# Performance work log

Hardware: AMD Instinct MI355X
Metric: run time of the kernel (lower is better)

## Reference

```python
import jax, jax.numpy as jnp
import numpy as np

NUM_HEADS = 16
BLOCK_SIZE = 64
NUM_RANDOM_BLOCKS = 2


def _make_sparse_mask(seq_len: int) -> np.ndarray:
    # Block-diagonal pattern: token i attends to tokens in the same block.
    blk = np.arange(seq_len) // BLOCK_SIZE
    mask = blk[:, None] == blk[None, :]
    # Random extra symmetric connections (torch.randint analogue, fixed seed).
    rng = np.random.default_rng(0)
    for _ in range(NUM_RANDOM_BLOCKS):
        i = int(rng.integers(0, seq_len))
        j = int(rng.integers(0, seq_len))
        mask[i, j] = True
        mask[j, i] = True
    return mask


def setup_inputs() -> dict:
    key = jax.random.key(0)
    B, S, E = 1, 4096, 1024
    ks = jax.random.split(key, 9)
    scale = 1.0 / np.sqrt(E)
    x = jax.random.normal(ks[0], (B, S, E), dtype=jnp.float32)
    Wq = jax.random.normal(ks[1], (E, E), dtype=jnp.float32) * scale
    bq = jax.random.normal(ks[2], (E,), dtype=jnp.float32) * 0.01
    Wk = jax.random.normal(ks[3], (E, E), dtype=jnp.float32) * scale
    bk = jax.random.normal(ks[4], (E,), dtype=jnp.float32) * 0.01
    Wv = jax.random.normal(ks[5], (E, E), dtype=jnp.float32) * scale
    bv = jax.random.normal(ks[6], (E,), dtype=jnp.float32) * 0.01
    Wo = jax.random.normal(ks[7], (E, E), dtype=jnp.float32) * scale
    bo = jax.random.normal(ks[8], (E,), dtype=jnp.float32) * 0.01
    sparse_mask = jnp.asarray(_make_sparse_mask(S))
    return {"x": x, "Wq": Wq, "bq": bq, "Wk": Wk, "bk": bk,
            "Wv": Wv, "bv": bv, "Wo": Wo, "bo": bo,
            "sparse_mask": sparse_mask}


def reference(x, Wq, bq, Wk, bk, Wv, bv, Wo, bo, sparse_mask):
    B, S, E = x.shape
    H = NUM_HEADS
    D = E // H
    # Linear projections (torch Linear: y = x @ W.T + b), split into heads.
    def proj(W, b):
        y = jnp.einsum('bse,fe->bsf', x, W) + b
        return y.reshape(B, S, H, D).transpose(0, 2, 1, 3)  # [B,H,S,D]
    Q = proj(Wq, bq)
    K = proj(Wk, bk)
    V = proj(Wv, bv)
    scores = jnp.einsum('bhqd,bhkd->bhqk', Q, K) / jnp.sqrt(jnp.float32(D))
    scores = jnp.where(sparse_mask, scores, jnp.float32(-1e9))
    attn = jax.nn.softmax(scores, axis=-1)  # dropout is identity in eval
    out = jnp.einsum('bhqk,bhkd->bhqd', attn, V)
    out = out.transpose(0, 2, 1, 3).reshape(B, S, E)
    out = jnp.einsum('bse,fe->bsf', out, Wo) + bo
    return out, attn
```

## Files before the change

### kernel.cpp

```cpp
#include <hip/hip_runtime.h>
#include <cstdint>
#include <cstddef>


#define S_LEN 4096
#define EMB   1024
#define NHEAD 16
#define HDIM  64
#define NBLK  64

typedef short bf16x8 __attribute__((ext_vector_type(8)));
typedef float f32x4  __attribute__((ext_vector_type(4)));

__global__ __launch_bounds__(256) void zero_fill(uint4* __restrict__ p, size_t n)
{
  size_t i = (size_t)blockIdx.x * blockDim.x + threadIdx.x;
  const size_t stride = (size_t)gridDim.x * blockDim.x;
  const uint4 z = {0u, 0u, 0u, 0u};
  for (; i < n; i += stride) p[i] = z;
}

__device__ __forceinline__ void split1(float v, unsigned short& h, unsigned short& l)
{
  const unsigned b  = __float_as_uint(v);
  const unsigned hr = (b + 0x8000u) >> 16;
  h = (unsigned short)hr;
  const float rem = v - __uint_as_float(hr << 16);
  l = (unsigned short)((__float_as_uint(rem) + 0x8000u) >> 16);
}

__global__ __launch_bounds__(256) void split_f32_bf16(
    const float* __restrict__ in, unsigned short* __restrict__ hi,
    unsigned short* __restrict__ lo, int n4)
{
  int i = blockIdx.x * blockDim.x + threadIdx.x;
  const int stride = gridDim.x * blockDim.x;
  for (; i < n4; i += stride) {
    const float4 v = ((const float4*)in)[i];
    ushort4 h, l;
    split1(v.x, h.x, l.x);
    split1(v.y, h.y, l.y);
    split1(v.z, h.z, l.z);
    split1(v.w, h.w, l.w);
    ((ushort4*)hi)[i] = h;
    ((ushort4*)lo)[i] = l;
  }
}

__global__ __launch_bounds__(256) void gemm_mfma_split(
    const unsigned short* __restrict__ Ahi, const unsigned short* __restrict__ Alo,
    const unsigned short* __restrict__ Bhi, const unsigned short* __restrict__ Blo,
    const float* __restrict__ bias, float* __restrict__ C, int M, int N, int K)
{
  __shared__ unsigned short sAh[128 * 40];
  __shared__ unsigned short sAl[128 * 40];
  __shared__ unsigned short sBh[128 * 40];
  __shared__ unsigned short sBl[128 * 40];

  const int tid  = threadIdx.x;
  const int m0   = blockIdx.y * 128;
  const int n0   = blockIdx.x * 128;
  const int lane = tid & 63;
  const int wave = tid >> 6;
  const int wr   = wave >> 1;
  const int wc   = wave & 1;
  const int r16  = lane & 15;
  const int kc   = lane >> 4;

  const int rt = tid >> 1;
  const int ht = tid & 1;
  const unsigned short* gAh = Ahi + (size_t)(m0 + rt) * K + ht * 16;
  const unsigned short* gAl = Alo + (size_t)(m0 + rt) * K + ht * 16;
  const unsigned short* gBh = Bhi + (size_t)(n0 + rt) * K + ht * 16;
  const unsigned short* gBl = Blo + (size_t)(n0 + rt) * K + ht * 16;
  const int lds_off = rt * 40 + ht * 16;

  f32x4 acc[4][4];
  #pragma unroll
  for (int i = 0; i < 4; ++i)
    #pragma unroll
    for (int j = 0; j < 4; ++j) acc[i][j] = (f32x4){0.f, 0.f, 0.f, 0.f};

  for (int k0 = 0; k0 < K; k0 += 32) {
    const uint4 vah0 = *(const uint4*)(gAh + k0);
    const uint4 vah1 = *(const uint4*)(gAh + k0 + 8);
    const uint4 val0 = *(const uint4*)(gAl + k0);
    const uint4 val1 = *(const uint4*)(gAl + k0 + 8);
    const uint4 vbh0 = *(const uint4*)(gBh + k0);
    const uint4 vbh1 = *(const uint4*)(gBh + k0 + 8);
    const uint4 vbl0 = *(const uint4*)(gBl + k0);
    const uint4 vbl1 = *(const uint4*)(gBl + k0 + 8);

    __syncthreads();
    *(uint4*)&sAh[lds_off]     = vah0;
    *(uint4*)&sAh[lds_off + 8] = vah1;
    *(uint4*)&sAl[lds_off]     = val0;
    *(uint4*)&sAl[lds_off + 8] = val1;
    *(uint4*)&sBh[lds_off]     = vbh0;
    *(uint4*)&sBh[lds_off + 8] = vbh1;
    *(uint4*)&sBl[lds_off]     = vbl0;
    *(uint4*)&sBl[lds_off + 8] = vbl1;
    __syncthreads();

    bf16x8 ah[4], al[4], bh[4], bl[4];
    #pragma unroll
    for (int mf = 0; mf < 4; ++mf) {
      const int row = wr * 64 + mf * 16 + r16;
      ah[mf] = *(const bf16x8*)&sAh[row * 40 + kc * 8];
      al[mf] = *(const bf16x8*)&sAl[row * 40 + kc * 8];
    }
    #pragma unroll
    for (int nf = 0; nf < 4; ++nf) {
      const int col = wc * 64 + nf * 16 + r16;
      bh[nf] = *(const bf16x8*)&sBh[col * 40 + kc * 8];
      bl[nf] = *(const bf16x8*)&sBl[col * 40 + kc * 8];
    }
    #pragma unroll
    for (int mf = 0; mf < 4; ++mf)
      #pragma unroll
      for (int nf = 0; nf < 4; ++nf) {
        acc[mf][nf] = __builtin_amdgcn_mfma_f32_16x16x32_bf16(ah[mf], bh[nf], acc[mf][nf], 0, 0, 0);
        acc[mf][nf] = __builtin_amdgcn_mfma_f32_16x16x32_bf16(ah[mf], bl[nf], acc[mf][nf], 0, 0, 0);
        acc[mf][nf] = __builtin_amdgcn_mfma_f32_16x16x32_bf16(al[mf], bh[nf], acc[mf][nf], 0, 0, 0);
      }
  }

  const int fq = lane >> 4;
  #pragma unroll
  for (int mf = 0; mf < 4; ++mf) {
    #pragma unroll
    for (int nf = 0; nf < 4; ++nf) {
      const int col = n0 + wc * 64 + nf * 16 + r16;
      const float bb = bias[col];
      #pragma unroll
      for (int v = 0; v < 4; ++v) {
        const int row = m0 + wr * 64 + mf * 16 + fq * 4 + v;
        C[(size_t)row * N + col] = acc[mf][nf][v] + bb;
      }
    }
  }
}

struct GemmPtrs {
  const float* W[3];
  const float* b[3];
  float* C[3];
};

__global__ __launch_bounds__(256) void gemm_bt_f32(const float* __restrict__ A,
                                                   GemmPtrs p, int M, int N, int K)
{
  const int z = blockIdx.z;
  const float* __restrict__ W    = p.W[z];
  const float* __restrict__ bias = p.b[z];
  float* __restrict__ C          = p.C[z];

  __shared__ float As[16][132];
  __shared__ float Bs[16][132];

  const int tid = threadIdx.x;
  const int tx = tid & 15;
  const int ty = tid >> 4;
  const int m0 = blockIdx.y * 128;
  const int n0 = blockIdx.x * 128;
  const int r0 = tid >> 2;
  const int c4 = tid & 3;

  const float* Ap  = A + (size_t)(m0 + r0) * K + c4 * 4;
  const float* Ap2 = Ap + (size_t)64 * K;
  const float* Wp  = W + (size_t)(n0 + r0) * K + c4 * 4;
  const float* Wp2 = Wp + (size_t)64 * K;

  float acc[8][8];
  #pragma unroll
  for (int i = 0; i < 8; ++i)
    #pragma unroll
    for (int j = 0; j < 8; ++j) acc[i][j] = 0.f;

  for (int k0 = 0; k0 < K; k0 += 16) {
    const float4 a0 = *(const float4*)(Ap  + k0);
    const float4 a1 = *(const float4*)(Ap2 + k0);
    const float4 w0 = *(const float4*)(Wp  + k0);
    const float4 w1 = *(const float4*)(Wp2 + k0);
    __syncthreads();
    As[c4*4+0][r0]    = a0.x; As[c4*4+1][r0]    = a0.y;
    As[c4*4+2][r0]    = a0.z; As[c4*4+3][r0]    = a0.w;
    As[c4*4+0][64+r0] = a1.x; As[c4*4+1][64+r0] = a1.y;
    As[c4*4+2][64+r0] = a1.z; As[c4*4+3][64+r0] = a1.w;
    Bs[c4*4+0][r0]    = w0.x; Bs[c4*4+1][r0]    = w0.y;
    Bs[c4*4+2][r0]    = w0.z; Bs[c4*4+3][r0]    = w0.w;
    Bs[c4*4+0][64+r0] = w1.x; Bs[c4*4+1][64+r0] = w1.y;
    Bs[c4*4+2][64+r0] = w1.z; Bs[c4*4+3][64+r0] = w1.w;
    __syncthreads();

    #pragma unroll
    for (int k = 0; k < 16; ++k) {
      const float4 av0 = *(const float4*)&As[k][ty*4];
      const float4 av1 = *(const float4*)&As[k][64 + ty*4];
      const float4 bv0 = *(const float4*)&Bs[k][tx*4];
      const float4 bv1 = *(const float4*)&Bs[k][64 + tx*4];
      const float av[8] = {av0.x, av0.y, av0.z, av0.w, av1.x, av1.y, av1.z, av1.w};
      const float bv[8] = {bv0.x, bv0.y, bv0.z, bv0.w, bv1.x, bv1.y, bv1.z, bv1.w};
      #pragma unroll
      for (int i = 0; i < 8; ++i)
        #pragma unroll
        for (int j = 0; j < 8; ++j)
          acc[i][j] += av[i] * bv[j];
    }
  }

  #pragma unroll
  for (int i = 0; i < 8; ++i) {
    const int row = m0 + (i >> 2) * 64 + ty * 4 + (i & 3);
    #pragma unroll
    for (int jg = 0; jg < 2; ++jg) {
      const int col = n0 + jg * 64 + tx * 4;
      const float4 bb = *(const float4*)&bias[col];
      float4 o;
      o.x = acc[i][jg*4+0] + bb.x;
      o.y = acc[i][jg*4+1] + bb.y;
      o.z = acc[i][jg*4+2] + bb.z;
      o.w = acc[i][jg*4+3] + bb.w;
      *(float4*)&C[(size_t)row * N + col] = o;
    }
  }
}

__global__ void probe_mode(const unsigned char* __restrict__ mask,
                           int* __restrict__ flags)
{
  if (blockIdx.x == 0 && threadIdx.x == 0) {
    int lsb = 0, msb3f = 0;
    #pragma unroll
    for (int t = 0; t < 8; ++t) {
      lsb   += (mask[64 + 4 * t] != 0) ? 1 : 0;
      msb3f += (mask[4 * t + 3] == 0x3f) ? 1 : 0;
    }
    flags[0] = (lsb >= 4 || msb3f >= 4) ? 1 : 0;
  }
}

__global__ void scan_mask(const unsigned char* __restrict__ mask,
                          const int* __restrict__ flags,
                          int* __restrict__ cnt, int* __restrict__ pairs)
{
  const int stride = gridDim.x * blockDim.x;
  const int t0 = blockIdx.x * blockDim.x + threadIdx.x;
  if (flags[0] == 0) {
    const uint4* m4 = (const uint4*)mask;
    const int n4 = (S_LEN * S_LEN) / 16;
    for (int i = t0; i < n4; i += stride) {
      const uint4 v = m4[i];
      if ((v.x | v.y | v.z | v.w) != 0u) {
        const unsigned int wv[4] = {v.x, v.y, v.z, v.w};
        #pragma unroll
        for (int wi = 0; wi < 4; ++wi)
          #pragma unroll
          for (int bi = 0; bi < 4; ++bi)
            if ((wv[wi] >> (8 * bi)) & 0xffu) {
              const int idx = i * 16 + wi * 4 + bi;
              const int r = idx >> 12, c = idx & 4095;
              if ((r >> 6) != (c >> 6)) {
                const int s = atomicAdd(cnt, 1);
                if (s < 64) pairs[s] = (r << 12) | c;
              }
            }
      }
    }
  } else {
    const uint4* m4 = (const uint4*)mask;
    const int n4 = (S_LEN * S_LEN) / 4;
    for (int i = t0; i < n4; i += stride) {
      const uint4 v = m4[i];
      if ((v.x | v.y | v.z | v.w) != 0u) {
        const unsigned int wv[4] = {v.x, v.y, v.z, v.w};
        #pragma unroll
        for (int wi = 0; wi < 4; ++wi)
          if (wv[wi] != 0u) {
            const int idx = i * 4 + wi;
            const int r = idx >> 12, c = idx & 4095;
            if ((r >> 6) != (c >> 6)) {
              const int s = atomicAdd(cnt, 1);
              if (s < 64) pairs[s] = (r << 12) | c;
            }
          }
      }
    }
  }
}

__global__ __launch_bounds__(256) void sparse_attn(
    const float* __restrict__ Qg, const float* __restrict__ Kg,
    const float* __restrict__ Vg, float* __restrict__ ctx,
    float* __restrict__ attn, const int* __restrict__ cntp,
    const int* __restrict__ pairs)
{
  __shared__ float Qs[64][64];
  __shared__ float Ks[64][68];
  __shared__ float Vs[64][64];
  __shared__ float P[64][64];
  __shared__ float exP[64][8];
  __shared__ int   exK[64][8];
  __shared__ int   exCnt[64];

  const int qb  = blockIdx.x;
  const int h   = blockIdx.y;
  const int s0  = qb * 64;
  const int tid = threadIdx.x;

  for (int f = tid; f < 64 * 16; f += 256) {
    const int r  = f >> 4;
    const int cc = (f & 15) * 4;
    const size_t g = (size_t)(s0 + r) * EMB + h * HDIM + cc;
    const float4 q4 = *(const float4*)(Qg + g);
    const float4 k4 = *(const float4*)(Kg + g);
    const float4 v4 = *(const float4*)(Vg + g);
    *(float4*)&Qs[r][cc] = q4;
    *(float4*)&Ks[r][cc] = k4;
    *(float4*)&Vs[r][cc] = v4;
  }
  __syncthreads();

  const int lane = tid & 63;
  const int wq   = tid >> 6;

  float kreg[64];
  #pragma unroll
  for (int d4 = 0; d4 < 16; ++d4) {
    const float4 kv = *(const float4*)&Ks[lane][d4 * 4];
    kreg[d4*4+0] = kv.x; kreg[d4*4+1] = kv.y;
    kreg[d4*4+2] = kv.z; kreg[d4*4+3] = kv.w;
  }

  #pragma unroll
  for (int it = 0; it < 16; ++it) {
    const int q = it * 4 + wq;
    float acc = 0.f;
    #pragma unroll
    for (int d4 = 0; d4 < 16; ++d4) {
      const float4 qv = *(const float4*)&Qs[q][d4 * 4];
      acc += qv.x * kreg[d4*4+0] + qv.y * kreg[d4*4+1]
           + qv.z * kreg[d4*4+2] + qv.w * kreg[d4*4+3];
    }
    const int sw = q & 15;
    P[q][(((lane >> 2) ^ sw) << 2) + (lane & 3)] = acc * 0.125f;
  }
  __syncthreads();

  if (tid < 64) {
    const int q   = tid;
    const int sw  = q & 15;
    const int row = s0 + q;
    float m = -1e30f;
    #pragma unroll
    for (int j = 0; j < 64; ++j) {
      const int pos = (((j >> 2) ^ sw) << 2) + (j & 3);
      m = fmaxf(m, P[q][pos]);
    }
    int ec = 0;
    int np = *cntp; if (np > 64) np = 64;
    for (int t = 0; t < np; ++t) {
      const int pr = pairs[t];
      if ((pr >> 12) == row) {
        const int pj = pr & 4095;
        const float* kp = Kg + (size_t)pj * EMB + h * HDIM;
        float s = 0.f;
        for (int d = 0; d < 64; ++d) s += Qs[q][d] * kp[d];
        s *= 0.125f;
        if (ec < 8) { exK[q][ec] = pj; exP[q][ec] = s; ++ec; }
      }
    }
    for (int e = 0; e < ec; ++e) m = fmaxf(m, exP[q][e]);
    float sum = 0.f;
    #pragma unroll
    for (int j = 0; j < 64; ++j) {
      const int pos = (((j >> 2) ^ sw) << 2) + (j & 3);
      const float v = expf(P[q][pos] - m);
      P[q][pos] = v;
      sum += v;
    }
    for (int e = 0; e < ec; ++e) { const float v = expf(exP[q][e] - m); exP[q][e] = v; sum += v; }
    const float inv = 1.0f / sum;
    #pragma unroll
    for (int j = 0; j < 64; ++j) {
      const int pos = (((j >> 2) ^ sw) << 2) + (j & 3);
      P[q][pos] *= inv;
    }
    for (int e = 0; e < ec; ++e) {
      const float pv = exP[q][e] * inv;
      exP[q][e] = pv;
      attn[((size_t)h * S_LEN + row) * S_LEN + exK[q][e]] = pv;
    }
    exCnt[q] = ec;
  }
  __syncthreads();

  float vcol[64];
  #pragma unroll
  for (int k = 0; k < 64; ++k) vcol[k] = Vs[k][lane];

  #pragma unroll
  for (int it = 0; it < 16; ++it) {
    const int q  = it * 4 + wq;
    const int sw = q & 15;
    float acc = 0.f;
    #pragma unroll
    for (int k4 = 0; k4 < 16; ++k4) {
      const float4 pv = *(const float4*)&P[q][(k4 ^ sw) << 2];
      acc += pv.x * vcol[k4*4+0] + pv.y * vcol[k4*4+1]
           + pv.z * vcol[k4*4+2] + pv.w * vcol[k4*4+3];
    }
    const int ec = exCnt[q];
    for (int e = 0; e < ec; ++e)
      acc += exP[q][e] * Vg[(size_t)exK[q][e] * EMB + h * HDIM + lane];
    ctx[(size_t)(s0 + q) * EMB + h * HDIM + lane] = acc;
  }

  for (int f = tid; f < 4096; f += 256) {
    const int q  = f >> 6;
    const int k  = f & 63;
    const int sw = q & 15;
    const int pos = (((k >> 2) ^ sw) << 2) + (k & 3);
    attn[((size_t)h * S_LEN + s0 + q) * S_LEN + s0 + k] = P[q][pos];
  }
}

extern "C" void kernel_launch(void* const* d_in, const int* in_sizes, int n_in,
                              void* d_out, int out_size, void* d_ws, size_t ws_size,
                              hipStream_t stream)
{
  (void)in_sizes; (void)n_in; (void)out_size;

  const float* x  = (const float*)d_in[0];
  const float* Wq = (const float*)d_in[1];
  const float* bq = (const float*)d_in[2];
  const float* Wk = (const float*)d_in[3];
  const float* bk = (const float*)d_in[4];
  const float* Wv = (const float*)d_in[5];
  const float* bv = (const float*)d_in[6];
  const float* Wo = (const float*)d_in[7];
  const float* bo = (const float*)d_in[8];
  const unsigned char* mask = (const unsigned char*)d_in[9];

  float* out  = (float*)d_out;
  float* attn = out + (size_t)S_LEN * EMB;

  char* ws = (char*)d_ws;
  const size_t MB = 1024 * 1024;
  float* Q   = (float*)(ws + 0 * MB);
  float* ctx = Q;
  float* Kb  = (float*)(ws + 16 * MB);
  float* Vb  = (float*)(ws + 32 * MB);

  const bool use_mfma = (ws_size >= 69 * MB);

  unsigned short* Ahi = (unsigned short*)(ws + 48 * MB);
  unsigned short* Alo = (unsigned short*)(ws + 56 * MB);
  unsigned short* Whi = (unsigned short*)(ws + 64 * MB);
  unsigned short* Wlo = (unsigned short*)(ws + 66 * MB);
  int* flags = (int*)(ws + (use_mfma ? 68 * MB : 48 * MB));
  int* cnt   = flags + 1;
  int* pairs = flags + 2;

  zero_fill<<<2048, 256, 0, stream>>>((uint4*)attn,
                                      (size_t)NHEAD * S_LEN * S_LEN / 4);
  hipMemsetAsync(flags, 0, (2 + 64) * sizeof(int), stream);

  probe_mode<<<1, 1, 0, stream>>>(mask, flags);
  scan_mask<<<2048, 256, 0, stream>>>(mask, flags, cnt, pairs);

  if (use_mfma) {
    const dim3 ggrid(EMB / 128, S_LEN / 128);
    split_f32_bf16<<<1024, 256, 0, stream>>>(x, Ahi, Alo, S_LEN * EMB / 4);
    split_f32_bf16<<<512, 256, 0, stream>>>(Wq, Whi, Wlo, EMB * EMB / 4);
    gemm_mfma_split<<<ggrid, 256, 0, stream>>>(Ahi, Alo, Whi, Wlo, bq, Q,  S_LEN, EMB, EMB);
    split_f32_bf16<<<512, 256, 0, stream>>>(Wk, Whi, Wlo, EMB * EMB / 4);
    gemm_mfma_split<<<ggrid, 256, 0, stream>>>(Ahi, Alo, Whi, Wlo, bk, Kb, S_LEN, EMB, EMB);
    split_f32_bf16<<<512, 256, 0, stream>>>(Wv, Whi, Wlo, EMB * EMB / 4);
    gemm_mfma_split<<<ggrid, 256, 0, stream>>>(Ahi, Alo, Whi, Wlo, bv, Vb, S_LEN, EMB, EMB);

    sparse_attn<<<dim3(NBLK, NHEAD), 256, 0, stream>>>(Q, Kb, Vb, ctx, attn, cnt, pairs);

    split_f32_bf16<<<1024, 256, 0, stream>>>(ctx, Ahi, Alo, S_LEN * EMB / 4);
    split_f32_bf16<<<512, 256, 0, stream>>>(Wo, Whi, Wlo, EMB * EMB / 4);
    gemm_mfma_split<<<ggrid, 256, 0, stream>>>(Ahi, Alo, Whi, Wlo, bo, out, S_LEN, EMB, EMB);
  } else {
    GemmPtrs pq;
    pq.W[0] = Wq; pq.W[1] = Wk; pq.W[2] = Wv;
    pq.b[0] = bq; pq.b[1] = bk; pq.b[2] = bv;
    pq.C[0] = Q;  pq.C[1] = Kb; pq.C[2] = Vb;
    gemm_bt_f32<<<dim3(EMB / 128, S_LEN / 128, 3), 256, 0, stream>>>(x, pq, S_LEN, EMB, EMB);

    sparse_attn<<<dim3(NBLK, NHEAD), 256, 0, stream>>>(Q, Kb, Vb, ctx, attn, cnt, pairs);

    GemmPtrs po;
    po.W[0] = Wo; po.W[1] = Wo; po.W[2] = Wo;
    po.b[0] = bo; po.b[1] = bo; po.b[2] = bo;
    po.C[0] = out; po.C[1] = out; po.C[2] = out;
    gemm_bt_f32<<<dim3(EMB / 128, S_LEN / 128, 1), 256, 0, stream>>>(ctx, po, S_LEN, EMB, EMB);
  }
}
```

Baseline: 1.436 ms.

## Batch QKV split-bf16 GEMMs, stage operands in attn buffer, nontemporal zero fill

Splits Wq, Wk and Wv in one batched kernel and runs all three projection GEMMs in a single z-batched launch. The bf16 hi/lo staging buffers now live in the still-unused attention output region and in the K/V scratch, so the MFMA path no longer depends on workspace size and the fp32 fallback GEMM is removed. The attention zero fill is moved after the projection GEMM so it overwrites that staging, and it now uses nontemporal stores. This cuts launch count and serialization and keeps the 1 GiB zero fill from polluting cache, at the cost of a strict ordering dependency between the staging buffers and the fill.

```diff
diff --git a/kernel.cpp b/kernel.cpp
--- a/kernel.cpp
+++ b/kernel.cpp
@@ -11,13 +11,14 @@
 
 typedef short bf16x8 __attribute__((ext_vector_type(8)));
 typedef float f32x4  __attribute__((ext_vector_type(4)));
-
-__global__ __launch_bounds__(256) void zero_fill(uint4* __restrict__ p, size_t n)
+typedef unsigned int u32x4 __attribute__((ext_vector_type(4)));
+
+__global__ __launch_bounds__(256) void zero_fill(u32x4* __restrict__ p, size_t n)
 {
   size_t i = (size_t)blockIdx.x * blockDim.x + threadIdx.x;
   const size_t stride = (size_t)gridDim.x * blockDim.x;
-  const uint4 z = {0u, 0u, 0u, 0u};
-  for (; i < n; i += stride) p[i] = z;
+  const u32x4 z = {0u, 0u, 0u, 0u};
+  for (; i < n; i += stride) __builtin_nontemporal_store(z, p + i);
 }
 
 __device__ __forceinline__ void split1(float v, unsigned short& h, unsigned short& l)
@@ -47,11 +48,49 @@
   }
 }
 
+struct SplitPtrs {
+  const float* in[3];
+  unsigned short* hi[3];
+  unsigned short* lo[3];
+};
+
+__global__ __launch_bounds__(256) void split3_f32_bf16(SplitPtrs p, int n4)
+{
+  const int z = blockIdx.z;
+  const float* __restrict__ in = p.in[z];
+  unsigned short* __restrict__ hi = p.hi[z];
+  unsigned short* __restrict__ lo = p.lo[z];
+  int i = blockIdx.x * blockDim.x + threadIdx.x;
+  const int stride = gridDim.x * blockDim.x;
+  for (; i < n4; i += stride) {
+    const float4 v = ((const float4*)in)[i];
+    ushort4 h, l;
+    split1(v.x, h.x, l.x);
+    split1(v.y, h.y, l.y);
+    split1(v.z, h.z, l.z);
+    split1(v.w, h.w, l.w);
+    ((ushort4*)hi)[i] = h;
+    ((ushort4*)lo)[i] = l;
+  }
+}
+
+struct GemmWPtrs {
+  const unsigned short* Wh[3];
+  const unsigned short* Wl[3];
+  const float* b[3];
+  float* C[3];
+};
+
 __global__ __launch_bounds__(256) void gemm_mfma_split(
     const unsigned short* __restrict__ Ahi, const unsigned short* __restrict__ Alo,
-    const unsigned short* __restrict__ Bhi, const unsigned short* __restrict__ Blo,
-    const float* __restrict__ bias, float* __restrict__ C, int M, int N, int K)
-{
+    GemmWPtrs p, int M, int N, int K)
+{
+  const int z = blockIdx.z;
+  const unsigned short* __restrict__ Bhi = p.Wh[z];
+  const unsigned short* __restrict__ Blo = p.Wl[z];
+  const float* __restrict__ bias = p.b[z];
+  float* __restrict__ C = p.C[z];
+
   __shared__ unsigned short sAh[128 * 40];
   __shared__ unsigned short sAl[128 * 40];
   __shared__ unsigned short sBh[128 * 40];
@@ -137,91 +176,6 @@
         const int row = m0 + wr * 64 + mf * 16 + fq * 4 + v;
         C[(size_t)row * N + col] = acc[mf][nf][v] + bb;
       }
-    }
-  }
-}
-
-struct GemmPtrs {
-  const float* W[3];
-  const float* b[3];
-  float* C[3];
-};
-
-__global__ __launch_bounds__(256) void gemm_bt_f32(const float* __restrict__ A,
-                                                   GemmPtrs p, int M, int N, int K)
-{
-  const int z = blockIdx.z;
-  const float* __restrict__ W    = p.W[z];
-  const float* __restrict__ bias = p.b[z];
-  float* __restrict__ C          = p.C[z];
-
-  __shared__ float As[16][132];
-  __shared__ float Bs[16][132];
-
-  const int tid = threadIdx.x;
-  const int tx = tid & 15;
-  const int ty = tid >> 4;
-  const int m0 = blockIdx.y * 128;
-  const int n0 = blockIdx.x * 128;
-  const int r0 = tid >> 2;
-  const int c4 = tid & 3;
-
-  const float* Ap  = A + (size_t)(m0 + r0) * K + c4 * 4;
-  const float* Ap2 = Ap + (size_t)64 * K;
-  const float* Wp  = W + (size_t)(n0 + r0) * K + c4 * 4;
-  const float* Wp2 = Wp + (size_t)64 * K;
-
-  float acc[8][8];
-  #pragma unroll
-  for (int i = 0; i < 8; ++i)
-    #pragma unroll
-    for (int j = 0; j < 8; ++j) acc[i][j] = 0.f;
-
-  for (int k0 = 0; k0 < K; k0 += 16) {
-    const float4 a0 = *(const float4*)(Ap  + k0);
-    const float4 a1 = *(const float4*)(Ap2 + k0);
-    const float4 w0 = *(const float4*)(Wp  + k0);
-    const float4 w1 = *(const float4*)(Wp2 + k0);
-    __syncthreads();
-    As[c4*4+0][r0]    = a0.x; As[c4*4+1][r0]    = a0.y;
-    As[c4*4+2][r0]    = a0.z; As[c4*4+3][r0]    = a0.w;
-    As[c4*4+0][64+r0] = a1.x; As[c4*4+1][64+r0] = a1.y;
-    As[c4*4+2][64+r0] = a1.z; As[c4*4+3][64+r0] = a1.w;
-    Bs[c4*4+0][r0]    = w0.x; Bs[c4*4+1][r0]    = w0.y;
-    Bs[c4*4+2][r0]    = w0.z; Bs[c4*4+3][r0]    = w0.w;
-    Bs[c4*4+0][64+r0] = w1.x; Bs[c4*4+1][64+r0] = w1.y;
-    Bs[c4*4+2][64+r0] = w1.z; Bs[c4*4+3][64+r0] = w1.w;
-    __syncthreads();
-
-    #pragma unroll
-    for (int k = 0; k < 16; ++k) {
-      const float4 av0 = *(const float4*)&As[k][ty*4];
-      const float4 av1 = *(const float4*)&As[k][64 + ty*4];
-      const float4 bv0 = *(const float4*)&Bs[k][tx*4];
-      const float4 bv1 = *(const float4*)&Bs[k][64 + tx*4];
-      const float av[8] = {av0.x, av0.y, av0.z, av0.w, av1.x, av1.y, av1.z, av1.w};
-      const float bv[8] = {bv0.x, bv0.y, bv0.z, bv0.w, bv1.x, bv1.y, bv1.z, bv1.w};
-      #pragma unroll
-      for (int i = 0; i < 8; ++i)
-        #pragma unroll
-        for (int j = 0; j < 8; ++j)
-          acc[i][j] += av[i] * bv[j];
-    }
-  }
-
-  #pragma unroll
-  for (int i = 0; i < 8; ++i) {
-    const int row = m0 + (i >> 2) * 64 + ty * 4 + (i & 3);
-    #pragma unroll
-    for (int jg = 0; jg < 2; ++jg) {
-      const int col = n0 + jg * 64 + tx * 4;
-      const float4 bb = *(const float4*)&bias[col];
-      float4 o;
-      o.x = acc[i][jg*4+0] + bb.x;
-      o.y = acc[i][jg*4+1] + bb.y;
-      o.z = acc[i][jg*4+2] + bb.z;
-      o.w = acc[i][jg*4+3] + bb.w;
-      *(float4*)&C[(size_t)row * N + col] = o;
     }
   }
 }
@@ -429,7 +383,7 @@
                               void* d_out, int out_size, void* d_ws, size_t ws_size,
                               hipStream_t stream)
 {
-  (void)in_sizes; (void)n_in; (void)out_size;
+  (void)in_sizes; (void)n_in; (void)out_size; (void)ws_size;
 
   const float* x  = (const float*)d_in[0];
   const float* Wq = (const float*)d_in[1];
@@ -451,52 +405,57 @@
   float* ctx = Q;
   float* Kb  = (float*)(ws + 16 * MB);
   float* Vb  = (float*)(ws + 32 * MB);
-
-  const bool use_mfma = (ws_size >= 69 * MB);
-
-  unsigned short* Ahi = (unsigned short*)(ws + 48 * MB);
-  unsigned short* Alo = (unsigned short*)(ws + 56 * MB);
-  unsigned short* Whi = (unsigned short*)(ws + 64 * MB);
-  unsigned short* Wlo = (unsigned short*)(ws + 66 * MB);
-  int* flags = (int*)(ws + (use_mfma ? 68 * MB : 48 * MB));
+  int* flags = (int*)(ws + 48 * MB);
   int* cnt   = flags + 1;
   int* pairs = flags + 2;
 
-  zero_fill<<<2048, 256, 0, stream>>>((uint4*)attn,
-                                      (size_t)NHEAD * S_LEN * S_LEN / 4);
-  hipMemsetAsync(flags, 0, (2 + 64) * sizeof(int), stream);
-
+  unsigned short* au = (unsigned short*)attn;
+  const size_t Msh = (size_t)1024 * 1024;
+  unsigned short* Ahi  = au;
+  unsigned short* Alo  = au + 4 * Msh;
+  unsigned short* Wqhi = au + 8 * Msh;
+  unsigned short* Wqlo = au + 9 * Msh;
+  unsigned short* Wkhi = au + 10 * Msh;
+  unsigned short* Wklo = au + 11 * Msh;
+  unsigned short* Wvhi = au + 12 * Msh;
+  unsigned short* Wvlo = au + 13 * Msh;
+
+  unsigned short* Chi  = (unsigned short*)Kb;
+  unsigned short* Clo  = (unsigned short*)Kb + 4 * Msh;
+  unsigned short* Wohi = (unsigned short*)Vb;
+  unsigned short* Wolo = (unsigned short*)Vb + Msh;
+
+  (void)hipMemsetAsync(flags, 0, (2 + 64) * sizeof(int), stream);
   probe_mode<<<1, 1, 0, stream>>>(mask, flags);
   scan_mask<<<2048, 256, 0, stream>>>(mask, flags, cnt, pairs);
 
-  if (use_mfma) {
-    const dim3 ggrid(EMB / 128, S_LEN / 128);
-    split_f32_bf16<<<1024, 256, 0, stream>>>(x, Ahi, Alo, S_LEN * EMB / 4);
-    split_f32_bf16<<<512, 256, 0, stream>>>(Wq, Whi, Wlo, EMB * EMB / 4);
-    gemm_mfma_split<<<ggrid, 256, 0, stream>>>(Ahi, Alo, Whi, Wlo, bq, Q,  S_LEN, EMB, EMB);
-    split_f32_bf16<<<512, 256, 0, stream>>>(Wk, Whi, Wlo, EMB * EMB / 4);
-    gemm_mfma_split<<<ggrid, 256, 0, stream>>>(Ahi, Alo, Whi, Wlo, bk, Kb, S_LEN, EMB, EMB);
-    split_f32_bf16<<<512, 256, 0, stream>>>(Wv, Whi, Wlo, EMB * EMB / 4);
-    gemm_mfma_split<<<ggrid, 256, 0, stream>>>(Ahi, Alo, Whi, Wlo, bv, Vb, S_LEN, EMB, EMB);
-
-    sparse_attn<<<dim3(NBLK, NHEAD), 256, 0, stream>>>(Q, Kb, Vb, ctx, attn, cnt, pairs);
-
-    split_f32_bf16<<<1024, 256, 0, stream>>>(ctx, Ahi, Alo, S_LEN * EMB / 4);
-    split_f32_bf16<<<512, 256, 0, stream>>>(Wo, Whi, Wlo, EMB * EMB / 4);
-    gemm_mfma_split<<<ggrid, 256, 0, stream>>>(Ahi, Alo, Whi, Wlo, bo, out, S_LEN, EMB, EMB);
-  } else {
-    GemmPtrs pq;
-    pq.W[0] = Wq; pq.W[1] = Wk; pq.W[2] = Wv;
-    pq.b[0] = bq; pq.b[1] = bk; pq.b[2] = bv;
-    pq.C[0] = Q;  pq.C[1] = Kb; pq.C[2] = Vb;
-    gemm_bt_f32<<<dim3(EMB / 128, S_LEN / 128, 3), 256, 0, stream>>>(x, pq, S_LEN, EMB, EMB);
-
-    sparse_attn<<<dim3(NBLK, NHEAD), 256, 0, stream>>>(Q, Kb, Vb, ctx, attn, cnt, pairs);
-
-    GemmPtrs po;
-    po.W[0] = Wo; po.W[1] = Wo; po.W[2] = Wo;
-    po.b[0] = bo; po.b[1] = bo; po.b[2] = bo;
-    po.C[0] = out; po.C[1] = out; po.C[2] = out;
-    gemm_bt_f32<<<dim3(EMB / 128, S_LEN / 128, 1), 256, 0, stream>>>(ctx, po, S_LEN, EMB, EMB);
-  }
-}
+  split_f32_bf16<<<1024, 256, 0, stream>>>(x, Ahi, Alo, S_LEN * EMB / 4);
+  SplitPtrs sp;
+  sp.in[0] = Wq; sp.in[1] = Wk; sp.in[2] = Wv;
+  sp.hi[0] = Wqhi; sp.hi[1] = Wkhi; sp.hi[2] = Wvhi;
+  sp.lo[0] = Wqlo; sp.lo[1] = Wklo; sp.lo[2] = Wvlo;
+  split3_f32_bf16<<<dim3(256, 1, 3), 256, 0, stream>>>(sp, EMB * EMB / 4);
+
+  GemmWPtrs pq;
+  pq.Wh[0] = Wqhi; pq.Wh[1] = Wkhi; pq.Wh[2] = Wvhi;
+  pq.Wl[0] = Wqlo; pq.Wl[1] = Wklo; pq.Wl[2] = Wvlo;
+  pq.b[0]  = bq;   pq.b[1]  = bk;   pq.b[2]  = bv;
+  pq.C[0]  = Q;    pq.C[1]  = Kb;   pq.C[2]  = Vb;
+  gemm_mfma_split<<<dim3(EMB / 128, S_LEN / 128, 3), 256, 0, stream>>>(
+      Ahi, Alo, pq, S_LEN, EMB, EMB);
+
+  zero_fill<<<2048, 256, 0, stream>>>((u32x4*)attn,
+                                      (size_t)NHEAD * S_LEN * S_LEN / 4);
+
+  sparse_attn<<<dim3(NBLK, NHEAD), 256, 0, stream>>>(Q, Kb, Vb, ctx, attn, cnt, pairs);
+
+  split_f32_bf16<<<1024, 256, 0, stream>>>(ctx, Chi, Clo, S_LEN * EMB / 4);
+  split_f32_bf16<<<256, 256, 0, stream>>>(Wo, Wohi, Wolo, EMB * EMB / 4);
+  GemmWPtrs po;
+  po.Wh[0] = Wohi; po.Wh[1] = Wohi; po.Wh[2] = Wohi;
+  po.Wl[0] = Wolo; po.Wl[1] = Wolo; po.Wl[2] = Wolo;
+  po.b[0]  = bo;   po.b[1]  = bo;   po.b[2]  = bo;
+  po.C[0]  = out;  po.C[1]  = out;  po.C[2]  = out;
+  gemm_mfma_split<<<dim3(EMB / 128, S_LEN / 128, 1), 256, 0, stream>>>(
+      Chi, Clo, po, S_LEN, EMB, EMB);
+}
```

New measurement: 1.375 ms. 1.04x faster.
